# Kernel tuning notes

Measured on AMD Instinct MI355X. Metric: run time of the kernel, lower is better.

The kernel has to match this reference:

```python
import jax, jax.numpy as jnp
import numpy as np

B, C, H, W = 2, 128, 48, 48
N = H * W
NQ = 25               # number of quantization bins (r2d2 default)
K_RELIABILITY = 0.5   # self.k
A = (NQ - 1) / 2.0    # quantizer slope over score range [-1, 1]
RADIUS = 4            # label window: [x-4 : x+5, y-4 : y+5]

# ---- quantizer line coefficients (r2d2 quantized AP) ----
# first half: q1 = -a*s + (a*min + [nq..1]);  special bin 0 -> constant 1
# second half: q2 =  a*s + ([2-nq..1] - a*min); special last bin -> constant 1
_W1 = jnp.full((NQ,), -A, jnp.float32).at[0].set(0.0)
_B1 = (jnp.arange(NQ, 0, -1, dtype=jnp.float32) - A).at[0].set(1.0)
_W2 = jnp.full((NQ,), A, jnp.float32).at[-1].set(0.0)
_B2 = (jnp.arange(2 - NQ, 2, dtype=jnp.float32) + A).at[-1].set(1.0)

# ---- ground-truth label matrix (static): pixel j positive for query i iff within 9x9 window ----
_row = np.arange(N) // W
_col = np.arange(N) % W
_L = ((np.abs(_row[:, None] - _row[None, :]) <= RADIUS) &
      (np.abs(_col[:, None] - _col[None, :]) <= RADIUS)).astype(np.float32)
LABEL = jnp.asarray(_L)  # (N, N)


def grid_sample_bilinear(img, grid):
    """torch.F.grid_sample: bilinear, zero padding, align_corners=False.
    img: (C, H, W); grid: (Hg, Wg, 2) in [-1, 1] -> out (C, Hg, Wg)."""
    Ci, Hi, Wi = img.shape
    ix = ((grid[..., 0] + 1.0) * Wi - 1.0) * 0.5
    iy = ((grid[..., 1] + 1.0) * Hi - 1.0) * 0.5
    x0 = jnp.floor(ix); y0 = jnp.floor(iy)
    wx1 = ix - x0; wy1 = iy - y0

    def gather(xi, yi):
        valid = (xi >= 0) & (xi < Wi) & (yi >= 0) & (yi < Hi)
        xc = jnp.clip(xi, 0, Wi - 1).astype(jnp.int32)
        yc = jnp.clip(yi, 0, Hi - 1).astype(jnp.int32)
        return img[:, yc, xc] * valid.astype(img.dtype)  # (C, Hg, Wg)

    return (gather(x0, y0) * (1 - wx1) * (1 - wy1)
            + gather(x0 + 1, y0) * wx1 * (1 - wy1)
            + gather(x0, y0 + 1) * (1 - wx1) * wy1
            + gather(x0 + 1, y0 + 1) * wx1 * wy1)


def quantized_ap(S, labels):
    """S: (N, M) similarity scores in [-1,1]; labels: (N, M) in {0,1}. Returns AP (N,)."""
    s = S[:, None, :]                                      # (N, 1, M)
    q1 = _W1[None, :, None] * s + _B1[None, :, None]        # (N, NQ, M)
    q2 = _W2[None, :, None] * s + _B2[None, :, None]
    q = jnp.maximum(jnp.minimum(q1, q2), 0.0)               # triangular bin weights
    nbs = q.sum(-1)                                         # (N, NQ) all counts per bin
    rec = jnp.einsum('ncm,nm->nc', q, labels)               # (N, NQ) positive counts per bin
    prec = jnp.cumsum(rec, -1) / (1e-16 + jnp.cumsum(nbs, -1))
    return (prec * rec).sum(-1) / rec.sum(-1)               # (N,)


def _loss_one(query_desc, db_desc, rel_map, g):
    db = grid_sample_bilinear(db_desc, g)                   # (C, H, W)
    Q = query_desc.reshape(C, N).T                          # (N, C)
    D = db.reshape(C, N).T                                  # (M=N, C)
    S = Q @ D.T                                             # (N, M) cosine scores
    ap = quantized_ap(S, LABEL)                             # (N,)
    r = rel_map.reshape(-1)                                 # (N,)
    return jnp.mean(1.0 - (ap * r + K_RELIABILITY * (1.0 - r)))


def setup_inputs() -> dict:
    key = jax.random.key(0)
    k1, k2, k3, k4 = jax.random.split(key, 4)
    d1 = jax.random.normal(k1, (B, C, H, W), jnp.float32)
    d1 = d1 / jnp.linalg.norm(d1, axis=1, keepdims=True)
    d2 = jax.random.normal(k2, (B, C, H, W), jnp.float32)
    d2 = d2 / jnp.linalg.norm(d2, axis=1, keepdims=True)
    rel = jax.random.uniform(k3, (B, 1, H, W), jnp.float32)
    grid = jax.random.uniform(k4, (B, H, W, 2), jnp.float32, minval=-1.0, maxval=1.0)
    return {"image1_descriptor": d1, "image2_descriptor": d2,
            "reliability": rel, "grid": grid}


def reference(image1_descriptor, image2_descriptor, reliability, grid):
    per_image = jax.vmap(_loss_one)(image1_descriptor, image2_descriptor,
                                    reliability[:, 0], grid)
    return per_image.mean()
```

## Files before the change

kernel.cpp:

```cpp
#include <hip/hip_runtime.h>
#include <hip/hip_bf16.h>

#define BB 2
#define CC 128
#define HH 48
#define WW 48
#define NN (HH*WW)
#define NBIN 26
#define QT 16
#define MT 64
#define MSPLIT 4
#define NTILES (NN/QT)
#define ITERS (NN/MSPLIT/MT)
#define HSTRIDE 27

typedef __bf16 bf16x8 __attribute__((ext_vector_type(8)));
typedef float  f32x4  __attribute__((ext_vector_type(4)));
typedef unsigned short u16;

static __device__ __forceinline__ u16 f2bf(float x) {
    __hip_bfloat16 h = __float2bfloat16(x);
    return __builtin_bit_cast(u16, h);
}

__global__ void k_transpose(const float* __restrict__ img1, u16* __restrict__ Qt) {
    int idx = blockIdx.x * 256 + threadIdx.x;
    int n = idx % NN;
    int c = (idx / NN) % CC;
    int b = idx / (NN * CC);
    Qt[((size_t)(b * NN + n)) * CC + c] = f2bf(img1[idx]);
}

#define CSPLIT 8
#define CCHUNK (CC/CSPLIT)
__global__ __launch_bounds__(256)
void k_gridsample(const float* __restrict__ img2, const float* __restrict__ grid,
                  u16* __restrict__ Dt) {
    int blk = blockIdx.x;
    int bm  = (blk >> 3) * 256 + threadIdx.x;
    int cc0 = (blk & 7) * CCHUNK;
    int b   = bm / NN;
    float gx = grid[bm * 2 + 0];
    float gy = grid[bm * 2 + 1];
    float ix = ((gx + 1.0f) * (float)WW - 1.0f) * 0.5f;
    float iy = ((gy + 1.0f) * (float)HH - 1.0f) * 0.5f;
    float x0f = floorf(ix), y0f = floorf(iy);
    float wx1 = ix - x0f, wy1 = iy - y0f;
    float wx0 = 1.0f - wx1, wy0 = 1.0f - wy1;
    int x0 = (int)x0f, y0 = (int)y0f;
    bool xv0 = (x0 >= 0) && (x0 < WW);
    bool xv1 = (x0 + 1 >= 0) && (x0 + 1 < WW);
    bool yv0 = (y0 >= 0) && (y0 < HH);
    bool yv1 = (y0 + 1 >= 0) && (y0 + 1 < HH);
    int x0c = min(max(x0, 0), WW - 1), x1c = min(max(x0 + 1, 0), WW - 1);
    int y0c = min(max(y0, 0), HH - 1), y1c = min(max(y0 + 1, 0), HH - 1);
    float w00 = (xv0 && yv0) ? wx0 * wy0 : 0.0f;
    float w01 = (xv1 && yv0) ? wx1 * wy0 : 0.0f;
    float w10 = (xv0 && yv1) ? wx0 * wy1 : 0.0f;
    float w11 = (xv1 && yv1) ? wx1 * wy1 : 0.0f;
    int p00 = y0c * WW + x0c, p01 = y0c * WW + x1c;
    int p10 = y1c * WW + x0c, p11 = y1c * WW + x1c;
    const float* im = img2 + (size_t)b * CC * NN + (size_t)cc0 * NN;
    u16 tmp[CCHUNK];
    #pragma unroll
    for (int c = 0; c < CCHUNK; ++c) {
        const float* pl = im + (size_t)c * NN;
        float v = pl[p00] * w00 + pl[p01] * w01 + pl[p10] * w10 + pl[p11] * w11;
        tmp[c] = f2bf(v);
    }
    uint4* dst = reinterpret_cast<uint4*>(Dt + (size_t)bm * CC + cc0);
    dst[0] = *reinterpret_cast<uint4*>(&tmp[0]);
    dst[1] = *reinterpret_cast<uint4*>(&tmp[8]);
}

__global__ __launch_bounds__(256)
void k_main(const u16* __restrict__ Qt, const u16* __restrict__ Dt,
            float* __restrict__ Hall, float* __restrict__ Hpos) {
    __shared__ u16  Qs[QT * 136];
    __shared__ u16  Ds[MT * 136];
    __shared__ float priv[256 * HSTRIDE];
    __shared__ float posh[QT * NBIN];

    int tid  = threadIdx.x;
    int bidx = blockIdx.x;
    int b      = bidx / (NTILES * MSPLIT);
    int rem    = bidx % (NTILES * MSPLIT);
    int ntile  = rem / MSPLIT;
    int msplit = rem % MSPLIT;
    int n0 = ntile * QT;

    for (int i = tid; i < 256 * HSTRIDE; i += 256) priv[i] = 0.0f;
    for (int i = tid; i < QT * NBIN; i += 256) posh[i] = 0.0f;
    {
        int row = tid >> 4, col = tid & 15;
        *reinterpret_cast<uint4*>(&Qs[row * 136 + col * 8]) =
            *reinterpret_cast<const uint4*>(Qt + ((size_t)(b * NN + n0 + row)) * CC + col * 8);
    }
    int lane = tid & 63, wave = tid >> 6, quad = lane >> 4, l15 = lane & 15;
    int q  = l15;
    int n  = n0 + q;
    int rn = n / WW, cn = n % WW;
    float* ph = &priv[tid * HSTRIDE];

    int mstart = msplit * (NN / MSPLIT);
    for (int it = 0; it < ITERS; ++it) {
        int m0 = mstart + it * MT;
        __syncthreads();
        #pragma unroll
        for (int k = 0; k < 4; ++k) {
            int idx = tid + k * 256;
            int row = idx >> 4, col = idx & 15;
            *reinterpret_cast<uint4*>(&Ds[row * 136 + col * 8]) =
                *reinterpret_cast<const uint4*>(Dt + ((size_t)(b * NN + m0 + row)) * CC + col * 8);
        }
        __syncthreads();

        f32x4 acc = {0.f, 0.f, 0.f, 0.f};
        #pragma unroll
        for (int kc = 0; kc < 4; ++kc) {
            bf16x8 av = *reinterpret_cast<const bf16x8*>(&Ds[(wave * 16 + l15) * 136 + kc * 32 + quad * 8]);
            bf16x8 bv = *reinterpret_cast<const bf16x8*>(&Qs[l15 * 136 + kc * 32 + quad * 8]);
            acc = __builtin_amdgcn_mfma_f32_16x16x32_bf16(av, bv, acc, 0, 0, 0);
        }

        int mb = m0 + wave * 16 + quad * 4;
        #pragma unroll
        for (int i = 0; i < 4; ++i) {
            float s  = acc[i];
            float t  = fminf(fmaxf(12.0f - 12.0f * s, 0.0f), 24.0f);
            float cf = floorf(t);
            float f  = t - cf;
            int   c0 = (int)cf;
            float h0 = ph[c0], h1 = ph[c0 + 1];
            ph[c0]     = h0 + (1.0f - f);
            ph[c0 + 1] = h1 + f;
            int m  = mb + i;
            int rm = m / WW, cm = m - rm * WW;
            int dr = rn - rm, dc = cn - cm;
            if ((unsigned)(dr + 4) <= 8u && (unsigned)(dc + 4) <= 8u) {
                atomicAdd(&posh[q * NBIN + c0],     1.0f - f);
                atomicAdd(&posh[q * NBIN + c0 + 1], f);
            }
        }
    }
    __syncthreads();
    for (int idx = tid; idx < QT * NBIN; idx += 256) {
        int qq = idx / NBIN, c = idx % NBIN;
        float s = 0.0f;
        #pragma unroll
        for (int j = 0; j < 16; ++j) s += priv[(j * 16 + qq) * HSTRIDE + c];
        size_t g = ((size_t)(b * NN + n0 + qq)) * NBIN + c;
        atomicAdd(&Hall[g], s);
        atomicAdd(&Hpos[g], posh[idx]);
    }
}

__global__ void k_finalize(const float* __restrict__ Hall, const float* __restrict__ Hpos,
                           const float* __restrict__ rel, float* __restrict__ out) {
    int gid = blockIdx.x * 256 + threadIdx.x;
    const float* ha = Hall + (size_t)gid * NBIN;
    const float* hp = Hpos + (size_t)gid * NBIN;
    float cumr = 0.f, cumn = 0.f, apn = 0.f, totr = 0.f;
    #pragma unroll
    for (int c2 = 0; c2 < 25; ++c2) {
        float r = hp[c2], a = ha[c2];
        cumr += r; cumn += a;
        apn  += (cumr / (1e-16f + cumn)) * r;
        totr += r;
    }
    float ap = apn / totr;
    float rl = rel[gid];
    float loss = 1.0f - (ap * rl + 0.5f * (1.0f - rl));

    for (int off = 32; off > 0; off >>= 1) loss += __shfl_down(loss, off, 64);
    __shared__ float wsum[4];
    int ln = threadIdx.x & 63, wv = threadIdx.x >> 6;
    if (ln == 0) wsum[wv] = loss;
    __syncthreads();
    if (threadIdx.x == 0) {
        float t = wsum[0] + wsum[1] + wsum[2] + wsum[3];
        atomicAdd(out, t * (1.0f / (float)(BB * NN)));
    }
}

extern "C" void kernel_launch(void* const* d_in, const int* in_sizes, int n_in,
                              void* d_out, int out_size, void* d_ws, size_t ws_size,
                              hipStream_t stream) {
    const float* img1 = (const float*)d_in[0];
    const float* img2 = (const float*)d_in[1];
    const float* rel  = (const float*)d_in[2];
    const float* grid = (const float*)d_in[3];

    char* ws = (char*)d_ws;
    const size_t qt_bytes   = (size_t)BB * NN * CC * sizeof(u16);
    const size_t hist_bytes = (size_t)BB * NN * NBIN * sizeof(float);
    u16*   Qt   = (u16*)ws;
    u16*   Dt   = (u16*)(ws + qt_bytes);
    float* Hall = (float*)(ws + 2 * qt_bytes);
    float* Hpos = (float*)(ws + 2 * qt_bytes + hist_bytes);

    hipMemsetAsync(d_out, 0, sizeof(float), stream);
    hipMemsetAsync(Hall, 0, 2 * hist_bytes, stream);

    k_transpose <<<(BB * CC * NN) / 256, 256, 0, stream>>>(img1, Qt);
    k_gridsample<<<(BB * NN / 256) * CSPLIT, 256, 0, stream>>>(img2, grid, Dt);
    k_main      <<<BB * NTILES * MSPLIT, 256, 0, stream>>>(Qt, Dt, Hall, Hpos);
    k_finalize  <<<(BB * NN) / 256, 256, 0, stream>>>(Hall, Hpos, rel, (float*)d_out);
}
```

Before: 111.2 us.

## Use 32x32 MFMA tiles, fuse prep kernels, write per-split partial histograms

The transpose and grid-sample kernels are merged into one prep kernel, and both memsets are removed: output zeroing moves into the prep kernel, and histograms become per-block partial slices that finalize sums instead of global atomics. The main kernel switches from 16x16x32 to 32x32x16 bf16 MFMA with 32 queries × 128 descriptors per tile and six M-splits. Each private histogram is now shared by two lanes through LDS atomics, which replaces per-thread read-modify-write. This cuts launch count and global atomic traffic, at the cost of extra LDS atomic contention and more partial-sum reads in finalize.

```diff
diff --git a/kernel.cpp b/kernel.cpp
--- a/kernel.cpp
+++ b/kernel.cpp
@@ -6,16 +6,17 @@
 #define HH 48
 #define WW 48
 #define NN (HH*WW)
-#define NBIN 26
-#define QT 16
-#define MT 64
-#define MSPLIT 4
+#define PB 26
+#define HST 27
+#define QT 32
+#define MT 128
+#define MSPLIT 6
 #define NTILES (NN/QT)
 #define ITERS (NN/MSPLIT/MT)
-#define HSTRIDE 27
+#define SLICE (QT*PB)
 
 typedef __bf16 bf16x8 __attribute__((ext_vector_type(8)));
-typedef float  f32x4  __attribute__((ext_vector_type(4)));
+typedef float  f32x16 __attribute__((ext_vector_type(16)));
 typedef unsigned short u16;
 
 static __device__ __forceinline__ u16 f2bf(float x) {
@@ -23,54 +24,57 @@
     return __builtin_bit_cast(u16, h);
 }
 
-__global__ void k_transpose(const float* __restrict__ img1, u16* __restrict__ Qt) {
-    int idx = blockIdx.x * 256 + threadIdx.x;
-    int n = idx % NN;
-    int c = (idx / NN) % CC;
-    int b = idx / (NN * CC);
-    Qt[((size_t)(b * NN + n)) * CC + c] = f2bf(img1[idx]);
-}
-
-#define CSPLIT 8
-#define CCHUNK (CC/CSPLIT)
 __global__ __launch_bounds__(256)
-void k_gridsample(const float* __restrict__ img2, const float* __restrict__ grid,
-                  u16* __restrict__ Dt) {
+void k_prep(const float* __restrict__ img1, const float* __restrict__ img2,
+            const float* __restrict__ grid, u16* __restrict__ Qt,
+            u16* __restrict__ Dt, float* __restrict__ out) {
     int blk = blockIdx.x;
-    int bm  = (blk >> 3) * 256 + threadIdx.x;
-    int cc0 = (blk & 7) * CCHUNK;
+    if (blk == 0 && threadIdx.x == 0) out[0] = 0.0f;
+    bool isg = blk >= 144;
+    int bb  = isg ? blk - 144 : blk;
+    int bm  = (bb >> 3) * 256 + threadIdx.x;
+    int cc0 = (bb & 7) * 16;
     int b   = bm / NN;
-    float gx = grid[bm * 2 + 0];
-    float gy = grid[bm * 2 + 1];
-    float ix = ((gx + 1.0f) * (float)WW - 1.0f) * 0.5f;
-    float iy = ((gy + 1.0f) * (float)HH - 1.0f) * 0.5f;
-    float x0f = floorf(ix), y0f = floorf(iy);
-    float wx1 = ix - x0f, wy1 = iy - y0f;
-    float wx0 = 1.0f - wx1, wy0 = 1.0f - wy1;
-    int x0 = (int)x0f, y0 = (int)y0f;
-    bool xv0 = (x0 >= 0) && (x0 < WW);
-    bool xv1 = (x0 + 1 >= 0) && (x0 + 1 < WW);
-    bool yv0 = (y0 >= 0) && (y0 < HH);
-    bool yv1 = (y0 + 1 >= 0) && (y0 + 1 < HH);
-    int x0c = min(max(x0, 0), WW - 1), x1c = min(max(x0 + 1, 0), WW - 1);
-    int y0c = min(max(y0, 0), HH - 1), y1c = min(max(y0 + 1, 0), HH - 1);
-    float w00 = (xv0 && yv0) ? wx0 * wy0 : 0.0f;
-    float w01 = (xv1 && yv0) ? wx1 * wy0 : 0.0f;
-    float w10 = (xv0 && yv1) ? wx0 * wy1 : 0.0f;
-    float w11 = (xv1 && yv1) ? wx1 * wy1 : 0.0f;
-    int p00 = y0c * WW + x0c, p01 = y0c * WW + x1c;
-    int p10 = y1c * WW + x0c, p11 = y1c * WW + x1c;
-    const float* im = img2 + (size_t)b * CC * NN + (size_t)cc0 * NN;
-    u16 tmp[CCHUNK];
-    #pragma unroll
-    for (int c = 0; c < CCHUNK; ++c) {
-        const float* pl = im + (size_t)c * NN;
-        float v = pl[p00] * w00 + pl[p01] * w01 + pl[p10] * w10 + pl[p11] * w11;
-        tmp[c] = f2bf(v);
-    }
-    uint4* dst = reinterpret_cast<uint4*>(Dt + (size_t)bm * CC + cc0);
-    dst[0] = *reinterpret_cast<uint4*>(&tmp[0]);
-    dst[1] = *reinterpret_cast<uint4*>(&tmp[8]);
+    int p   = bm - b * NN;
+    u16 tmp[16];
+    if (!isg) {
+        const float* im = img1 + (size_t)b * CC * NN + (size_t)cc0 * NN;
+        #pragma unroll
+        for (int c = 0; c < 16; ++c) tmp[c] = f2bf(im[(size_t)c * NN + p]);
+        uint4* dst = reinterpret_cast<uint4*>(Qt + (size_t)bm * CC + cc0);
+        dst[0] = *reinterpret_cast<uint4*>(&tmp[0]);
+        dst[1] = *reinterpret_cast<uint4*>(&tmp[8]);
+    } else {
+        float gx = grid[bm * 2 + 0];
+        float gy = grid[bm * 2 + 1];
+        float ix = ((gx + 1.0f) * (float)WW - 1.0f) * 0.5f;
+        float iy = ((gy + 1.0f) * (float)HH - 1.0f) * 0.5f;
+        float x0f = floorf(ix), y0f = floorf(iy);
+        float wx1 = ix - x0f, wy1 = iy - y0f;
+        float wx0 = 1.0f - wx1, wy0 = 1.0f - wy1;
+        int x0 = (int)x0f, y0 = (int)y0f;
+        bool xv0 = (x0 >= 0) && (x0 < WW);
+        bool xv1 = (x0 + 1 >= 0) && (x0 + 1 < WW);
+        bool yv0 = (y0 >= 0) && (y0 < HH);
+        bool yv1 = (y0 + 1 >= 0) && (y0 + 1 < HH);
+        int x0c = min(max(x0, 0), WW - 1), x1c = min(max(x0 + 1, 0), WW - 1);
+        int y0c = min(max(y0, 0), HH - 1), y1c = min(max(y0 + 1, 0), HH - 1);
+        float w00 = (xv0 && yv0) ? wx0 * wy0 : 0.0f;
+        float w01 = (xv1 && yv0) ? wx1 * wy0 : 0.0f;
+        float w10 = (xv0 && yv1) ? wx0 * wy1 : 0.0f;
+        float w11 = (xv1 && yv1) ? wx1 * wy1 : 0.0f;
+        int p00 = y0c * WW + x0c, p01 = y0c * WW + x1c;
+        int p10 = y1c * WW + x0c, p11 = y1c * WW + x1c;
+        const float* im = img2 + (size_t)b * CC * NN + (size_t)cc0 * NN;
+        #pragma unroll
+        for (int c = 0; c < 16; ++c) {
+            const float* pl = im + (size_t)c * NN;
+            tmp[c] = f2bf(pl[p00] * w00 + pl[p01] * w01 + pl[p10] * w10 + pl[p11] * w11);
+        }
+        uint4* dst = reinterpret_cast<uint4*>(Dt + (size_t)bm * CC + cc0);
+        dst[0] = *reinterpret_cast<uint4*>(&tmp[0]);
+        dst[1] = *reinterpret_cast<uint4*>(&tmp[8]);
+    }
 }
 
 __global__ __launch_bounds__(256)
@@ -78,92 +82,103 @@
             float* __restrict__ Hall, float* __restrict__ Hpos) {
     __shared__ u16  Qs[QT * 136];
     __shared__ u16  Ds[MT * 136];
-    __shared__ float priv[256 * HSTRIDE];
-    __shared__ float posh[QT * NBIN];
+    __shared__ float priv[128 * HST];
+    __shared__ float posh[QT * PB];
 
     int tid  = threadIdx.x;
     int bidx = blockIdx.x;
-    int b      = bidx / (NTILES * MSPLIT);
-    int rem    = bidx % (NTILES * MSPLIT);
-    int ntile  = rem / MSPLIT;
-    int msplit = rem % MSPLIT;
+    int b     = bidx / (NTILES * MSPLIT);
+    int rem   = bidx % (NTILES * MSPLIT);
+    int ntile = rem / MSPLIT;
+    int ms    = rem % MSPLIT;
     int n0 = ntile * QT;
 
-    for (int i = tid; i < 256 * HSTRIDE; i += 256) priv[i] = 0.0f;
-    for (int i = tid; i < QT * NBIN; i += 256) posh[i] = 0.0f;
-    {
-        int row = tid >> 4, col = tid & 15;
+    for (int i = tid; i < 128 * HST; i += 256) priv[i] = 0.0f;
+    for (int i = tid; i < QT * PB; i += 256) posh[i] = 0.0f;
+    #pragma unroll
+    for (int k2 = 0; k2 < 2; ++k2) {
+        int idx = tid + k2 * 256;
+        int row = idx >> 4, col = idx & 15;
         *reinterpret_cast<uint4*>(&Qs[row * 136 + col * 8]) =
             *reinterpret_cast<const uint4*>(Qt + ((size_t)(b * NN + n0 + row)) * CC + col * 8);
     }
-    int lane = tid & 63, wave = tid >> 6, quad = lane >> 4, l15 = lane & 15;
-    int q  = l15;
+    int lane = tid & 63, wave = tid >> 6, h = lane >> 5, l31 = lane & 31;
+    int q  = l31;
     int n  = n0 + q;
     int rn = n / WW, cn = n % WW;
-    float* ph = &priv[tid * HSTRIDE];
-
-    int mstart = msplit * (NN / MSPLIT);
+    float* ph = &priv[(wave * 32 + l31) * HST];
+
+    int mstart = ms * (NN / MSPLIT);
     for (int it = 0; it < ITERS; ++it) {
         int m0 = mstart + it * MT;
         __syncthreads();
         #pragma unroll
-        for (int k = 0; k < 4; ++k) {
-            int idx = tid + k * 256;
+        for (int k2 = 0; k2 < 8; ++k2) {
+            int idx = tid + k2 * 256;
             int row = idx >> 4, col = idx & 15;
             *reinterpret_cast<uint4*>(&Ds[row * 136 + col * 8]) =
                 *reinterpret_cast<const uint4*>(Dt + ((size_t)(b * NN + m0 + row)) * CC + col * 8);
         }
         __syncthreads();
 
-        f32x4 acc = {0.f, 0.f, 0.f, 0.f};
-        #pragma unroll
-        for (int kc = 0; kc < 4; ++kc) {
-            bf16x8 av = *reinterpret_cast<const bf16x8*>(&Ds[(wave * 16 + l15) * 136 + kc * 32 + quad * 8]);
-            bf16x8 bv = *reinterpret_cast<const bf16x8*>(&Qs[l15 * 136 + kc * 32 + quad * 8]);
-            acc = __builtin_amdgcn_mfma_f32_16x16x32_bf16(av, bv, acc, 0, 0, 0);
-        }
-
-        int mb = m0 + wave * 16 + quad * 4;
-        #pragma unroll
-        for (int i = 0; i < 4; ++i) {
-            float s  = acc[i];
-            float t  = fminf(fmaxf(12.0f - 12.0f * s, 0.0f), 24.0f);
+        f32x16 acc = {0.f,0.f,0.f,0.f,0.f,0.f,0.f,0.f,0.f,0.f,0.f,0.f,0.f,0.f,0.f,0.f};
+        #pragma unroll
+        for (int kc = 0; kc < 8; ++kc) {
+            bf16x8 av = *reinterpret_cast<const bf16x8*>(&Ds[(wave * 32 + l31) * 136 + kc * 16 + h * 8]);
+            bf16x8 bv = *reinterpret_cast<const bf16x8*>(&Qs[l31 * 136 + kc * 16 + h * 8]);
+            acc = __builtin_amdgcn_mfma_f32_32x32x16_bf16(av, bv, acc, 0, 0, 0);
+        }
+
+        int mbase = m0 + wave * 32 + 4 * h;
+        #pragma unroll
+        for (int r = 0; r < 16; ++r) {
+            int mloc = (r & 3) + 8 * (r >> 2);
+            float s  = acc[r];
+            float t  = fminf(fmaxf(fmaf(-12.0f, s, 12.0f), 0.0f), 24.0f);
             float cf = floorf(t);
             float f  = t - cf;
             int   c0 = (int)cf;
-            float h0 = ph[c0], h1 = ph[c0 + 1];
-            ph[c0]     = h0 + (1.0f - f);
-            ph[c0 + 1] = h1 + f;
-            int m  = mb + i;
+            atomicAdd(&ph[c0],     1.0f - f);
+            atomicAdd(&ph[c0 + 1], f);
+            int m  = mbase + mloc;
             int rm = m / WW, cm = m - rm * WW;
             int dr = rn - rm, dc = cn - cm;
             if ((unsigned)(dr + 4) <= 8u && (unsigned)(dc + 4) <= 8u) {
-                atomicAdd(&posh[q * NBIN + c0],     1.0f - f);
-                atomicAdd(&posh[q * NBIN + c0 + 1], f);
+                atomicAdd(&posh[q * PB + c0],     1.0f - f);
+                atomicAdd(&posh[q * PB + c0 + 1], f);
             }
         }
     }
     __syncthreads();
-    for (int idx = tid; idx < QT * NBIN; idx += 256) {
-        int qq = idx / NBIN, c = idx % NBIN;
-        float s = 0.0f;
-        #pragma unroll
-        for (int j = 0; j < 16; ++j) s += priv[(j * 16 + qq) * HSTRIDE + c];
-        size_t g = ((size_t)(b * NN + n0 + qq)) * NBIN + c;
-        atomicAdd(&Hall[g], s);
-        atomicAdd(&Hpos[g], posh[idx]);
-    }
-}
-
-__global__ void k_finalize(const float* __restrict__ Hall, const float* __restrict__ Hpos,
-                           const float* __restrict__ rel, float* __restrict__ out) {
+    float* oa = Hall + (size_t)bidx * SLICE;
+    float* op = Hpos + (size_t)bidx * SLICE;
+    for (int idx = tid; idx < SLICE; idx += 256) {
+        int c = idx >> 5, qq = idx & 31;
+        float s2 = priv[qq * HST + c] + priv[(32 + qq) * HST + c]
+                 + priv[(64 + qq) * HST + c] + priv[(96 + qq) * HST + c];
+        oa[idx] = s2;
+        op[idx] = posh[qq * PB + c];
+    }
+}
+
+__global__ __launch_bounds__(256)
+void k_finalize(const float* __restrict__ Hall, const float* __restrict__ Hpos,
+                const float* __restrict__ rel, float* __restrict__ out) {
     int gid = blockIdx.x * 256 + threadIdx.x;
-    const float* ha = Hall + (size_t)gid * NBIN;
-    const float* hp = Hpos + (size_t)gid * NBIN;
+    int b = gid / NN, nloc = gid % NN;
+    int ntile = nloc >> 5, qq = nloc & 31;
+    size_t base = ((size_t)(b * NTILES + ntile) * MSPLIT) * SLICE + qq;
+    const float* ha = Hall + base;
+    const float* hp = Hpos + base;
     float cumr = 0.f, cumn = 0.f, apn = 0.f, totr = 0.f;
     #pragma unroll
-    for (int c2 = 0; c2 < 25; ++c2) {
-        float r = hp[c2], a = ha[c2];
+    for (int c = 0; c < 25; ++c) {
+        float a = 0.f, r = 0.f;
+        #pragma unroll
+        for (int s = 0; s < MSPLIT; ++s) {
+            a += ha[(size_t)s * SLICE + c * 32];
+            r += hp[(size_t)s * SLICE + c * 32];
+        }
         cumr += r; cumn += a;
         apn  += (cumr / (1e-16f + cumn)) * r;
         totr += r;
@@ -193,17 +208,13 @@
 
     char* ws = (char*)d_ws;
     const size_t qt_bytes   = (size_t)BB * NN * CC * sizeof(u16);
-    const size_t hist_bytes = (size_t)BB * NN * NBIN * sizeof(float);
+    const size_t part_bytes = (size_t)BB * NTILES * MSPLIT * SLICE * sizeof(float);
     u16*   Qt   = (u16*)ws;
     u16*   Dt   = (u16*)(ws + qt_bytes);
     float* Hall = (float*)(ws + 2 * qt_bytes);
-    float* Hpos = (float*)(ws + 2 * qt_bytes + hist_bytes);
-
-    hipMemsetAsync(d_out, 0, sizeof(float), stream);
-    hipMemsetAsync(Hall, 0, 2 * hist_bytes, stream);
-
-    k_transpose <<<(BB * CC * NN) / 256, 256, 0, stream>>>(img1, Qt);
-    k_gridsample<<<(BB * NN / 256) * CSPLIT, 256, 0, stream>>>(img2, grid, Dt);
-    k_main      <<<BB * NTILES * MSPLIT, 256, 0, stream>>>(Qt, Dt, Hall, Hpos);
-    k_finalize  <<<(BB * NN) / 256, 256, 0, stream>>>(Hall, Hpos, rel, (float*)d_out);
-}
+    float* Hpos = (float*)(ws + 2 * qt_bytes + part_bytes);
+
+    k_prep    <<<288, 256, 0, stream>>>(img1, img2, grid, Qt, Dt, (float*)d_out);
+    k_main    <<<BB * NTILES * MSPLIT, 256, 0, stream>>>(Qt, Dt, Hall, Hpos);
+    k_finalize<<<(BB * NN) / 256, 256, 0, stream>>>(Hall, Hpos, rel, (float*)d_out);
+}
```

After: 280.0 us. +151.7%, slower.
